# Kernel optimization log

Measured on AMD Instinct MI355X. Metric: run time of the kernel, lower is better.

The kernel has to match this reference:

```python
import jax, jax.numpy as jnp
import numpy as np
import math

D_MODEL = 768
NUM_HEADS = 12
SPARSITY = 0.7


def setup_inputs() -> dict:
    key = jax.random.key(0)
    ks = jax.random.split(key, 9)
    B, S, D = 2, 2048, D_MODEL
    scale = 1.0 / math.sqrt(D)  # xavier-ish
    inp = {
        "x": jax.random.normal(ks[0], (B, S, D), dtype=jnp.float32),
        "Wq": jax.random.normal(ks[1], (D, D), dtype=jnp.float32) * scale,
        "bq": jnp.zeros((D,), dtype=jnp.float32),
        "Wk": jax.random.normal(ks[2], (D, D), dtype=jnp.float32) * scale,
        "bk": jnp.zeros((D,), dtype=jnp.float32),
        "Wv": jax.random.normal(ks[3], (D, D), dtype=jnp.float32) * scale,
        "bv": jnp.zeros((D,), dtype=jnp.float32),
        "Wo": jax.random.normal(ks[4], (D, D), dtype=jnp.float32) * scale,
        "bo": jnp.zeros((D,), dtype=jnp.float32),
    }
    return inp


def reference(x, Wq, bq, Wk, bk, Wv, bv, Wo, bo):
    B, S, D = x.shape
    H = NUM_HEADS
    hd = D // H
    k_keep = max(1, int((1.0 - SPARSITY) * S))

    # projections (nn.Linear: x @ W.T + b), split into heads -> [B,H,S,hd]
    q = (x @ Wq.T + bq).reshape(B, S, H, hd).transpose(0, 2, 1, 3)
    k = (x @ Wk.T + bk).reshape(B, S, H, hd).transpose(0, 2, 1, 3)
    v = (x @ Wv.T + bv).reshape(B, S, H, hd).transpose(0, 2, 1, 3)

    # dense scores [B,H,S,S]
    scores = jnp.einsum("bhqd,bhkd->bhqk", q, k) / math.sqrt(hd)

    # per-row top-k sparsification (training path of the torch module)
    _, topk_idx = jax.lax.top_k(scores, k_keep)  # [B,H,S,k]
    bi = jnp.arange(B)[:, None, None, None]
    hi = jnp.arange(H)[None, :, None, None]
    si = jnp.arange(S)[None, None, :, None]
    keep = jnp.zeros(scores.shape, dtype=bool).at[bi, hi, si, topk_idx].set(True)
    scores = jnp.where(keep, scores, jnp.float32(-1e9))

    attn = jax.nn.softmax(scores, axis=-1)
    out = jnp.einsum("bhqk,bhkd->bhqd", attn, v)  # [B,H,S,hd]
    out = out.transpose(0, 2, 1, 3).reshape(B, S, D)
    return out @ Wo.T + bo
```

## Files before the change

kernel.cpp:

```cpp
#include <hip/hip_runtime.h>
#include <math.h>

#define B_ 2
#define S_ 2048
#define D_ 768
#define H_ 12
#define HD_ 64
#define KKEEP 614
#define M_ (B_*S_)
#define KD_ 768
#define SRW 2072

typedef __attribute__((ext_vector_type(8))) short bf8;
typedef __attribute__((ext_vector_type(4))) float f4;

__device__ __forceinline__ unsigned short f2bf(float f) {
    unsigned u = __float_as_uint(f);
    u += 0x7FFF + ((u >> 16) & 1);
    return (unsigned short)(u >> 16);
}
__device__ __forceinline__ float bf2f(unsigned short h) {
    return __uint_as_float((unsigned)h << 16);
}
__device__ __forceinline__ unsigned ord16(unsigned short h) {
    return (h & 0x8000u) ? ((~(unsigned)h) & 0xFFFFu) : ((unsigned)h | 0x8000u);
}
__device__ __forceinline__ unsigned short inv16(unsigned o) {
    return (unsigned short)((o & 0x8000u) ? (o & 0x7FFFu) : ((~o) & 0xFFFFu));
}

__global__ void split_kernel(const float* __restrict__ src,
                             unsigned short* __restrict__ hi,
                             unsigned short* __restrict__ lo, int n) {
    int i = blockIdx.x * blockDim.x + threadIdx.x;
    if (i >= n) return;
    float f = src[i];
    unsigned short h = f2bf(f);
    hi[i] = h;
    lo[i] = f2bf(f - bf2f(h));
}

__global__ void split_w_kernel(const float* __restrict__ w0, const float* __restrict__ w1,
                               const float* __restrict__ w2, const float* __restrict__ w3,
                               unsigned short* __restrict__ hi,
                               unsigned short* __restrict__ lo) {
    const int which = blockIdx.y;
    const float* src = which == 0 ? w0 : (which == 1 ? w1 : (which == 2 ? w2 : w3));
    int i = blockIdx.x * blockDim.x + threadIdx.x;
    size_t o = (size_t)which * (D_ * D_) + i;
    float f = src[i];
    unsigned short h = f2bf(f);
    hi[o] = h;
    lo[o] = f2bf(f - bf2f(h));
}

__global__ __launch_bounds__(256)
void gemm_qkv(const unsigned short* __restrict__ Ahi, const unsigned short* __restrict__ Alo,
              const unsigned short* __restrict__ Wch, const unsigned short* __restrict__ Wcl,
              const float* __restrict__ bq, const float* __restrict__ bk,
              const float* __restrict__ bv,
              unsigned short* __restrict__ Qh, unsigned short* __restrict__ Ql,
              unsigned short* __restrict__ Kh, unsigned short* __restrict__ Vth) {
    __shared__ unsigned short Ah[128][32], Al[128][32], Bh[64][32], Bl[64][32];
    const int bm = blockIdx.x * 128, bnG = blockIdx.y * 64;
    const int which = blockIdx.y / 12;
    const int bn = bnG - which * 768;
    const float* bias = which == 0 ? bq : (which == 1 ? bk : bv);
    const int tid = threadIdx.x, lane = tid & 63, wave = tid >> 6;
    const int col = lane & 15, quad = lane >> 4;

    f4 acc[2][4];
#pragma unroll
    for (int mi = 0; mi < 2; ++mi)
#pragma unroll
        for (int ni = 0; ni < 4; ++ni) { f4 z = {0.f,0.f,0.f,0.f}; acc[mi][ni] = z; }

    for (int kt = 0; kt < KD_; kt += 32) {
        __syncthreads();
#pragma unroll
        for (int c = 0; c < 2; ++c) {
            int idx = c * 256 + tid;
            int row = idx >> 2, ko = (idx & 3) * 8;
            *(uint4*)&Ah[row][ko] = *(const uint4*)&Ahi[(size_t)(bm + row) * KD_ + kt + ko];
            *(uint4*)&Al[row][ko] = *(const uint4*)&Alo[(size_t)(bm + row) * KD_ + kt + ko];
        }
        {
            int row = tid >> 2, ko = (tid & 3) * 8;
            *(uint4*)&Bh[row][ko] = *(const uint4*)&Wch[(size_t)(bnG + row) * KD_ + kt + ko];
            *(uint4*)&Bl[row][ko] = *(const uint4*)&Wcl[(size_t)(bnG + row) * KD_ + kt + ko];
        }
        __syncthreads();

        bf8 af[2][2], wf[4][2];
#pragma unroll
        for (int mi = 0; mi < 2; ++mi) {
            int r = wave * 32 + mi * 16 + col;
            af[mi][0] = *(const bf8*)&Ah[r][quad * 8];
            af[mi][1] = *(const bf8*)&Al[r][quad * 8];
        }
#pragma unroll
        for (int ni = 0; ni < 4; ++ni) {
            int r = ni * 16 + col;
            wf[ni][0] = *(const bf8*)&Bh[r][quad * 8];
            wf[ni][1] = *(const bf8*)&Bl[r][quad * 8];
        }
#pragma unroll
        for (int mi = 0; mi < 2; ++mi)
#pragma unroll
            for (int ni = 0; ni < 4; ++ni) {
                acc[mi][ni] = __builtin_amdgcn_mfma_f32_16x16x32_bf16(af[mi][0], wf[ni][0], acc[mi][ni], 0, 0, 0);
                acc[mi][ni] = __builtin_amdgcn_mfma_f32_16x16x32_bf16(af[mi][1], wf[ni][0], acc[mi][ni], 0, 0, 0);
                acc[mi][ni] = __builtin_amdgcn_mfma_f32_16x16x32_bf16(af[mi][0], wf[ni][1], acc[mi][ni], 0, 0, 0);
            }
    }

    float bvv[4];
#pragma unroll
    for (int ni = 0; ni < 4; ++ni) bvv[ni] = bias[bn + ni * 16 + col];
#pragma unroll
    for (int mi = 0; mi < 2; ++mi)
#pragma unroll
        for (int ni = 0; ni < 4; ++ni)
#pragma unroll
            for (int r = 0; r < 4; ++r) {
                int m = bm + wave * 32 + mi * 16 + quad * 4 + r;
                int n = bn + ni * 16 + col;
                float v = acc[mi][ni][r] + bvv[ni];
                int b = m >> 11, s = m & 2047, h = n >> 6, d = n & 63;
                unsigned short hh = f2bf(v);
                if (which == 0) {
                    size_t idx = (((size_t)b * H_ + h) * S_ + s) * HD_ + d;
                    Qh[idx] = hh;
                    Ql[idx] = f2bf(v - bf2f(hh));
                } else if (which == 1) {
                    Kh[(((size_t)b * H_ + h) * S_ + s) * HD_ + d] = hh;
                } else {
                    Vth[(((size_t)b * H_ + h) * HD_ + d) * S_ + s] = hh;
                }
            }
}

__global__ __launch_bounds__(256)
void gemm_o(const unsigned short* __restrict__ Ahi, const unsigned short* __restrict__ Alo,
            const unsigned short* __restrict__ Whi, const unsigned short* __restrict__ Wlo,
            const float* __restrict__ bias, float* __restrict__ outf) {
    __shared__ unsigned short Ah[128][32], Al[128][32], Bh[64][32], Bl[64][32];
    const int bm = blockIdx.x * 128, bn = blockIdx.y * 64;
    const int tid = threadIdx.x, lane = tid & 63, wave = tid >> 6;
    const int col = lane & 15, quad = lane >> 4;

    f4 acc[2][4];
#pragma unroll
    for (int mi = 0; mi < 2; ++mi)
#pragma unroll
        for (int ni = 0; ni < 4; ++ni) { f4 z = {0.f,0.f,0.f,0.f}; acc[mi][ni] = z; }

    for (int kt = 0; kt < KD_; kt += 32) {
        __syncthreads();
#pragma unroll
        for (int c = 0; c < 2; ++c) {
            int idx = c * 256 + tid;
            int row = idx >> 2, ko = (idx & 3) * 8;
            *(uint4*)&Ah[row][ko] = *(const uint4*)&Ahi[(size_t)(bm + row) * KD_ + kt + ko];
            *(uint4*)&Al[row][ko] = *(const uint4*)&Alo[(size_t)(bm + row) * KD_ + kt + ko];
        }
        {
            int row = tid >> 2, ko = (tid & 3) * 8;
            *(uint4*)&Bh[row][ko] = *(const uint4*)&Whi[(size_t)(bn + row) * KD_ + kt + ko];
            *(uint4*)&Bl[row][ko] = *(const uint4*)&Wlo[(size_t)(bn + row) * KD_ + kt + ko];
        }
        __syncthreads();

        bf8 af[2][2], wf[4][2];
#pragma unroll
        for (int mi = 0; mi < 2; ++mi) {
            int r = wave * 32 + mi * 16 + col;
            af[mi][0] = *(const bf8*)&Ah[r][quad * 8];
            af[mi][1] = *(const bf8*)&Al[r][quad * 8];
        }
#pragma unroll
        for (int ni = 0; ni < 4; ++ni) {
            int r = ni * 16 + col;
            wf[ni][0] = *(const bf8*)&Bh[r][quad * 8];
            wf[ni][1] = *(const bf8*)&Bl[r][quad * 8];
        }
#pragma unroll
        for (int mi = 0; mi < 2; ++mi)
#pragma unroll
            for (int ni = 0; ni < 4; ++ni) {
                acc[mi][ni] = __builtin_amdgcn_mfma_f32_16x16x32_bf16(af[mi][0], wf[ni][0], acc[mi][ni], 0, 0, 0);
                acc[mi][ni] = __builtin_amdgcn_mfma_f32_16x16x32_bf16(af[mi][1], wf[ni][0], acc[mi][ni], 0, 0, 0);
                acc[mi][ni] = __builtin_amdgcn_mfma_f32_16x16x32_bf16(af[mi][0], wf[ni][1], acc[mi][ni], 0, 0, 0);
            }
    }

    float bvv[4];
#pragma unroll
    for (int ni = 0; ni < 4; ++ni) bvv[ni] = bias[bn + ni * 16 + col];
#pragma unroll
    for (int mi = 0; mi < 2; ++mi)
#pragma unroll
        for (int ni = 0; ni < 4; ++ni)
#pragma unroll
            for (int r = 0; r < 4; ++r) {
                int m = bm + wave * 32 + mi * 16 + quad * 4 + r;
                int n = bn + ni * 16 + col;
                outf[(size_t)m * D_ + n] = acc[mi][ni][r] + bvv[ni];
            }
}

__global__ __launch_bounds__(1024, 8)
void attn_kernel(const unsigned short* __restrict__ Qhi, const unsigned short* __restrict__ Qlo,
                 const unsigned short* __restrict__ Khi,
                 const unsigned short* __restrict__ Vthi,
                 unsigned short* __restrict__ AOhi, unsigned short* __restrict__ AOlo) {
    const int bid = blockIdx.x;
    const int xcd = bid & 7, sub = (bid >> 3) % 3, tile = bid / 24;
    const int bh = xcd * 3 + sub;
    const int b = bh / H_, h = bh % H_;
    const int q0 = tile * 16;
    const int tid = threadIdx.x, lane = tid & 63, wave = tid >> 6;
    const int col = lane & 15, quad = lane >> 4;

    __shared__ __align__(16) unsigned char arena[16 * 4144];
    unsigned short* scB = (unsigned short*)arena;
    float (*osum)[16][64] = (float (*)[16][64])arena;
    __shared__ float linv[16];

    const size_t qbase = ((size_t)bh * S_ + q0 + col) * HD_;
    bf8 qh0 = *(const bf8*)&Qhi[qbase + quad * 8];
    bf8 qh1 = *(const bf8*)&Qhi[qbase + 32 + quad * 8];
    bf8 ql0 = *(const bf8*)&Qlo[qbase + quad * 8];
    bf8 ql1 = *(const bf8*)&Qlo[qbase + 32 + quad * 8];

    const size_t kbb = (size_t)bh * S_ * HD_;
#pragma unroll 1
    for (int t = 0; t < 8; ++t) {
        const size_t kr = kbb + (size_t)(wave * 128 + t * 16 + col) * HD_;
        bf8 kh0 = *(const bf8*)&Khi[kr + quad * 8];
        bf8 kh1 = *(const bf8*)&Khi[kr + 32 + quad * 8];
        f4 a = {0.f, 0.f, 0.f, 0.f};
        a = __builtin_amdgcn_mfma_f32_16x16x32_bf16(qh0, kh0, a, 0, 0, 0);
        a = __builtin_amdgcn_mfma_f32_16x16x32_bf16(qh1, kh1, a, 0, 0, 0);
        a = __builtin_amdgcn_mfma_f32_16x16x32_bf16(ql0, kh0, a, 0, 0, 0);
        a = __builtin_amdgcn_mfma_f32_16x16x32_bf16(ql1, kh1, a, 0, 0, 0);
#pragma unroll
        for (int r = 0; r < 4; ++r)
            scB[(quad * 4 + r) * SRW + wave * 128 + t * 16 + col] =
                (unsigned short)ord16(f2bf(a[r] * 0.125f));
    }
    __syncthreads();

    unsigned* rowp = (unsigned*)(arena + wave * 4144);
    unsigned kv[16];
#pragma unroll
    for (int j = 0; j < 16; ++j) kv[j] = rowp[lane + 64 * j];

    unsigned mo = 0;
#pragma unroll
    for (int j = 0; j < 16; ++j) {
        unsigned hi = kv[j] >> 16, lo = kv[j] & 0xFFFFu;
        mo = mo > hi ? mo : hi;
        mo = mo > lo ? mo : lo;
    }
#pragma unroll
    for (int off = 1; off < 64; off <<= 1) {
        unsigned v = __shfl_xor((int)mo, off, 64);
        mo = mo > v ? mo : v;
    }
    unsigned T = 0;
#pragma unroll 1
    for (int bit = 15; bit >= 0; --bit) {
        unsigned cand = T | (1u << bit);
        int cnt = 0;
#pragma unroll
        for (int j = 0; j < 16; ++j)
            cnt += (int)((kv[j] >> 16) >= cand) + (int)((kv[j] & 0xFFFFu) >= cand);
#pragma unroll
        for (int off = 1; off < 64; off <<= 1) cnt += __shfl_xor(cnt, off, 64);
        if (cnt >= KKEEP) T = cand;
    }
    const float m = bf2f(inv16(mo));

    float ls = 0.f;
#pragma unroll 1
    for (int j = 0; j < 16; ++j) {
        unsigned v = kv[j];
        unsigned lo = v & 0xFFFFu, hi = v >> 16;
        float wl = (lo >= T) ? __expf(bf2f(inv16(lo)) - m) : 0.f;
        float wh = (hi >= T) ? __expf(bf2f(inv16(hi)) - m) : 0.f;
        ls += wl + wh;
        rowp[lane + 64 * j] = (unsigned)f2bf(wl) | ((unsigned)f2bf(wh) << 16);
    }
#pragma unroll
    for (int off = 1; off < 64; off <<= 1) ls += __shfl_xor(ls, off, 64);
    if (lane == 0) linv[wave] = 1.f / ls;
    __syncthreads();

    f4 od[4];
#pragma unroll
    for (int dt = 0; dt < 4; ++dt) { f4 z = {0.f,0.f,0.f,0.f}; od[dt] = z; }
    const size_t vbb = (size_t)bh * HD_ * S_;
#pragma unroll 1
    for (int c = 0; c < 4; ++c) {
        bf8 ph = *(const bf8*)&scB[col * SRW + wave * 128 + c * 32 + quad * 8];
        const size_t sbase = (size_t)(wave * 128 + c * 32 + quad * 8);
#pragma unroll
        for (int dt = 0; dt < 4; ++dt) {
            bf8 vh = *(const bf8*)&Vthi[vbb + (size_t)(dt * 16 + col) * S_ + sbase];
            od[dt] = __builtin_amdgcn_mfma_f32_16x16x32_bf16(ph, vh, od[dt], 0, 0, 0);
        }
    }
    __syncthreads();
    if (wave < 8) {
#pragma unroll
        for (int dt = 0; dt < 4; ++dt)
#pragma unroll
            for (int r = 0; r < 4; ++r)
                osum[wave][quad * 4 + r][dt * 16 + col] = od[dt][r];
    }
    __syncthreads();
    if (wave >= 8) {
#pragma unroll
        for (int dt = 0; dt < 4; ++dt)
#pragma unroll
            for (int r = 0; r < 4; ++r)
                osum[wave - 8][quad * 4 + r][dt * 16 + col] += od[dt][r];
    }
    __syncthreads();

    {
        int q = tid >> 6, d = tid & 63;
        float s = 0.f;
#pragma unroll
        for (int w = 0; w < 8; ++w) s += osum[w][q][d];
        s *= linv[q];
        size_t idx = ((size_t)b * S_ + q0 + q) * D_ + h * HD_ + d;
        unsigned short hh = f2bf(s);
        AOhi[idx] = hh;
        AOlo[idx] = f2bf(s - bf2f(hh));
    }
}

extern "C" void kernel_launch(void* const* d_in, const int* in_sizes, int n_in,
                              void* d_out, int out_size, void* d_ws, size_t ws_size,
                              hipStream_t stream) {
    const float* x  = (const float*)d_in[0];
    const float* Wq = (const float*)d_in[1];
    const float* bq = (const float*)d_in[2];
    const float* Wk = (const float*)d_in[3];
    const float* bk = (const float*)d_in[4];
    const float* Wv = (const float*)d_in[5];
    const float* bv = (const float*)d_in[6];
    const float* Wo = (const float*)d_in[7];
    const float* bo = (const float*)d_in[8];
    float* out = (float*)d_out;

    const size_t NP = (size_t)M_ * D_;
    const size_t NW = (size_t)D_ * D_;
    unsigned short* p = (unsigned short*)d_ws;
    unsigned short* xhi = p;  p += NP;
    unsigned short* xlo = p;  p += NP;
    unsigned short* Wch = p;  p += 4 * NW;
    unsigned short* Wcl = p;  p += 4 * NW;
    unsigned short* Qh  = p;  p += NP;  unsigned short* Ql  = p;  p += NP;
    unsigned short* Kh  = p;  p += NP;
    unsigned short* Vth = p;  p += NP;
    unsigned short* AOh = xhi;
    unsigned short* AOl = xlo;

    split_kernel<<<(int)(NP / 256), 256, 0, stream>>>(x, xhi, xlo, (int)NP);
    {
        dim3 gw((unsigned)(NW / 256), 4);
        split_w_kernel<<<gw, 256, 0, stream>>>(Wq, Wk, Wv, Wo, Wch, Wcl);
    }

    {
        dim3 g(M_ / 128, 36);
        gemm_qkv<<<g, 256, 0, stream>>>(xhi, xlo, Wch, Wcl, bq, bk, bv,
                                        Qh, Ql, Kh, Vth);
    }

    attn_kernel<<<(S_ / 16) * B_ * H_, 1024, 0, stream>>>(Qh, Ql, Kh, Vth, AOh, AOl);

    {
        dim3 g(M_ / 128, D_ / 64);
        gemm_o<<<g, 256, 0, stream>>>(AOh, AOl, Wch + 3 * NW, Wcl + 3 * NW, bo, out);
    }
}
```

Baseline: 439.9 us.

## Speed up top-k threshold search with ballot counts and fold score scale into Q

The per-bit radix-select count now uses wave ballots and popcount on pre-shifted 32-bit keys, replacing the per-lane compare-and-shuffle reduction. The 1/sqrt(hd) factor moves into the Q projection epilogue, and a fused float-to-ordered-bf16 conversion replaces the separate round-then-order steps. The cross-wave output reduction drops one barrier by having all 16 waves write their own partial-sum slot and summing 16 slots. This relies on the partial-sum buffer having room for 16 slots. The exp is now computed unconditionally and masked afterwards, which removes a branch but spends extra transcendental work on discarded entries.

Measured after the change: 430.3 us. 2.2% less time.

```diff
diff --git a/kernel.cpp b/kernel.cpp
--- a/kernel.cpp
+++ b/kernel.cpp
@@ -22,11 +22,15 @@
 __device__ __forceinline__ float bf2f(unsigned short h) {
     return __uint_as_float((unsigned)h << 16);
 }
-__device__ __forceinline__ unsigned ord16(unsigned short h) {
-    return (h & 0x8000u) ? ((~(unsigned)h) & 0xFFFFu) : ((unsigned)h | 0x8000u);
-}
-__device__ __forceinline__ unsigned short inv16(unsigned o) {
-    return (unsigned short)((o & 0x8000u) ? (o & 0x7FFFu) : ((~o) & 0xFFFFu));
+__device__ __forceinline__ unsigned f2ord16(float f) {
+    unsigned u = __float_as_uint(f);
+    unsigned o32 = u ^ ((unsigned)((int)u >> 31) | 0x80000000u);
+    return (o32 + 0x7FFFu + ((o32 >> 16) & 1u)) >> 16;
+}
+__device__ __forceinline__ float ord16_to_f(unsigned o16) {
+    unsigned o = o16 << 16;
+    unsigned mask = 0x80000000u | ~(unsigned)((int)o >> 31);
+    return __uint_as_float((o ^ mask) & 0xFFFF0000u);
 }
 
 __global__ void split_kernel(const float* __restrict__ src,
@@ -126,6 +130,7 @@
                 int m = bm + wave * 32 + mi * 16 + quad * 4 + r;
                 int n = bn + ni * 16 + col;
                 float v = acc[mi][ni][r] + bvv[ni];
+                if (which == 0) v *= 0.125f;
                 int b = m >> 11, s = m & 2047, h = n >> 6, d = n & 63;
                 unsigned short hh = f2bf(v);
                 if (which == 0) {
@@ -247,48 +252,53 @@
 #pragma unroll
         for (int r = 0; r < 4; ++r)
             scB[(quad * 4 + r) * SRW + wave * 128 + t * 16 + col] =
-                (unsigned short)ord16(f2bf(a[r] * 0.125f));
+                (unsigned short)f2ord16(a[r]);
     }
     __syncthreads();
 
     unsigned* rowp = (unsigned*)(arena + wave * 4144);
-    unsigned kv[16];
+    unsigned kv[16], kvs[16];
 #pragma unroll
     for (int j = 0; j < 16; ++j) kv[j] = rowp[lane + 64 * j];
-
-    unsigned mo = 0;
+#pragma unroll
+    for (int j = 0; j < 16; ++j) kvs[j] = kv[j] << 16;
+
+    unsigned Mhi = 0, Mlo = 0;
 #pragma unroll
     for (int j = 0; j < 16; ++j) {
-        unsigned hi = kv[j] >> 16, lo = kv[j] & 0xFFFFu;
-        mo = mo > hi ? mo : hi;
-        mo = mo > lo ? mo : lo;
-    }
+        Mhi = kv[j]  > Mhi ? kv[j]  : Mhi;
+        Mlo = kvs[j] > Mlo ? kvs[j] : Mlo;
+    }
+    unsigned mo = (Mhi >> 16) > (Mlo >> 16) ? (Mhi >> 16) : (Mlo >> 16);
 #pragma unroll
     for (int off = 1; off < 64; off <<= 1) {
         unsigned v = __shfl_xor((int)mo, off, 64);
         mo = mo > v ? mo : v;
     }
+    const float m = ord16_to_f(mo);
+
     unsigned T = 0;
 #pragma unroll 1
     for (int bit = 15; bit >= 0; --bit) {
-        unsigned cand = T | (1u << bit);
+        unsigned candh = (T | (1u << bit)) << 16;
         int cnt = 0;
 #pragma unroll
-        for (int j = 0; j < 16; ++j)
-            cnt += (int)((kv[j] >> 16) >= cand) + (int)((kv[j] & 0xFFFFu) >= cand);
-#pragma unroll
-        for (int off = 1; off < 64; off <<= 1) cnt += __shfl_xor(cnt, off, 64);
-        if (cnt >= KKEEP) T = cand;
-    }
-    const float m = bf2f(inv16(mo));
+        for (int j = 0; j < 16; ++j) {
+            cnt += __popcll(__ballot(kv[j]  >= candh));
+            cnt += __popcll(__ballot(kvs[j] >= candh));
+        }
+        if (cnt >= KKEEP) T |= (1u << bit);
+    }
 
     float ls = 0.f;
 #pragma unroll 1
     for (int j = 0; j < 16; ++j) {
-        unsigned v = kv[j];
-        unsigned lo = v & 0xFFFFu, hi = v >> 16;
-        float wl = (lo >= T) ? __expf(bf2f(inv16(lo)) - m) : 0.f;
-        float wh = (hi >= T) ? __expf(bf2f(inv16(hi)) - m) : 0.f;
+        unsigned lo16 = kv[j] & 0xFFFFu;
+        unsigned hi16 = kv[j] >> 16;
+        float wl = __expf(ord16_to_f(lo16) - m);
+        float wh = __expf(ord16_to_f(hi16) - m);
+        wl = (lo16 >= T) ? wl : 0.f;
+        wh = (hi16 >= T) ? wh : 0.f;
         ls += wl + wh;
         rowp[lane + 64 * j] = (unsigned)f2bf(wl) | ((unsigned)f2bf(wh) << 16);
     }
@@ -312,28 +322,18 @@
         }
     }
     __syncthreads();
-    if (wave < 8) {
-#pragma unroll
-        for (int dt = 0; dt < 4; ++dt)
-#pragma unroll
-            for (int r = 0; r < 4; ++r)
-                osum[wave][quad * 4 + r][dt * 16 + col] = od[dt][r];
-    }
-    __syncthreads();
-    if (wave >= 8) {
-#pragma unroll
-        for (int dt = 0; dt < 4; ++dt)
-#pragma unroll
-            for (int r = 0; r < 4; ++r)
-                osum[wave - 8][quad * 4 + r][dt * 16 + col] += od[dt][r];
-    }
+#pragma unroll
+    for (int dt = 0; dt < 4; ++dt)
+#pragma unroll
+        for (int r = 0; r < 4; ++r)
+            osum[wave][quad * 4 + r][dt * 16 + col] = od[dt][r];
     __syncthreads();
 
     {
         int q = tid >> 6, d = tid & 63;
         float s = 0.f;
 #pragma unroll
-        for (int w = 0; w < 8; ++w) s += osum[w][q][d];
+        for (int w = 0; w < 16; ++w) s += osum[w][q][d];
         s *= linv[q];
         size_t idx = ((size_t)b * S_ + q0 + q) * D_ + h * HD_ + d;
         unsigned short hh = f2bf(s);
```
